# Kernel optimization log

Hardware: AMD Instinct MI355X
Metric: run time of the kernel (lower is better)

Reference implementation:

```python
import jax, jax.numpy as jnp
import numpy as np

DIM = 512
BATCH = 4096
STEPS = 30
GOVERNOR_RANK = 321
LAMBDA_0 = 15.045
RANK_EPS = 1e-5


def setup_inputs() -> dict:
    key = jax.random.key(0)
    kx, kw = jax.random.split(key)
    x = jax.random.normal(kx, (BATCH, DIM), dtype=jnp.float32)
    # nn.Linear(dim, dim) with weight ~ N(0, (1.2/sqrt(dim))^2), bias = 0.01
    std = 1.2 / float(np.sqrt(DIM))
    W = jax.random.normal(kw, (DIM, DIM), dtype=jnp.float32) * std
    b = jnp.full((DIM,), 0.01, dtype=jnp.float32)
    return {"x": x, "W": W, "b": b}


def reference(x, W, b):
    # is_governed = governor_rank < 1e6 -> True, so the amplify branch is dead code.
    norm_factor = float(np.sqrt(BATCH * DIM))
    k = min(BATCH, DIM)  # number of singular values from thin SVD
    idx = jnp.arange(k)

    def step(h, _):
        h = h @ W.T + b  # [B, D]
        U, S, Vh = jnp.linalg.svd(h, full_matrices=False)  # U:[B,k] S:[k] Vh:[k,D]
        current_rank = jnp.sum(S > RANK_EPS)
        trunc = current_rank > GOVERNOR_RANK
        S = jnp.where(trunc & (idx >= GOVERNOR_RANK), 0.0, S)
        l1_sings = jnp.sum(S) / norm_factor  # recorded BEFORE rescale, as in torch
        scale = jnp.where(l1_sings > LAMBDA_0,
                          LAMBDA_0 * norm_factor / jnp.sum(S), 1.0)
        h = (U * (S * scale)) @ Vh  # reconstruct U diag(S) Vh
        return h, l1_sings

    _, activations = jax.lax.scan(step, x, None, length=STEPS)
    return activations  # [STEPS] l1 singular-value sums, matching the returned list
```

## Files before the change

### kernel.cpp

```cpp
#include <hip/hip_runtime.h>
#include <math.h>

#define DIM 512
#define BATCH 4096
#define NSTEPS 30
#define KEEP 321

#define S_BETA 0
#define S_SCALE 1
#define S_VTV 4
#define S_SC 5

#define TDG 32
#define MTAIL 96

__device__ __forceinline__ double wred(double v) {
#pragma unroll
  for (int o = 32; o > 0; o >>= 1) v += __shfl_down(v, (unsigned)o, 64);
  return v;
}

__device__ __forceinline__ void stg(double* p, double v) {
  __hip_atomic_store(p, v, __ATOMIC_RELAXED, __HIP_MEMORY_SCOPE_AGENT);
}
__device__ __forceinline__ double ldg_(const double* p) {
  return __hip_atomic_load(p, __ATOMIC_RELAXED, __HIP_MEMORY_SCOPE_AGENT);
}

__device__ __forceinline__ void gbar2(unsigned* __restrict__ flags, unsigned& gen) {
  gen++;
  const unsigned target = gen;
  __syncthreads();
  if (threadIdx.x == 0) {
    __threadfence();
    __hip_atomic_store(flags + (size_t)blockIdx.x * 32, target, __ATOMIC_RELAXED, __HIP_MEMORY_SCOPE_AGENT);
  }
  if (threadIdx.x < 64) {
    bool ok = ((int)threadIdx.x >= TDG);
    while (!__all(ok)) {
      if (!ok) {
        unsigned v = __hip_atomic_load(flags + (size_t)threadIdx.x * 32, __ATOMIC_RELAXED, __HIP_MEMORY_SCOPE_AGENT);
        ok = (v >= target);
      }
    }
    __threadfence();
  }
  __syncthreads();
}

__device__ __forceinline__ void gbarf(unsigned* __restrict__ flags, unsigned& gen) {
  gen++;
  const unsigned target = gen;
  __syncthreads();
  if (threadIdx.x == 0) {
    __hip_atomic_store(flags + (size_t)blockIdx.x * 32, target, __ATOMIC_RELAXED, __HIP_MEMORY_SCOPE_AGENT);
  }
  if (threadIdx.x < 64) {
    bool ok = ((int)threadIdx.x >= TDG);
    while (!__all(ok)) {
      if (!ok) {
        unsigned v = __hip_atomic_load(flags + (size_t)threadIdx.x * 32, __ATOMIC_RELAXED, __HIP_MEMORY_SCOPE_AGENT);
        ok = (v >= target);
      }
    }
    asm volatile("" ::: "memory");
  }
  __syncthreads();
}


__global__ __launch_bounds__(256) void k_cast(const float* __restrict__ W, const float* __restrict__ b,
                                              double* __restrict__ Wd, double* __restrict__ bd,
                                              unsigned* __restrict__ cflags) {
  int idx = blockIdx.x * 256 + threadIdx.x;
  if (idx < DIM * DIM) Wd[idx] = (double)W[idx];
  if (idx < DIM) bd[idx] = (double)b[idx];
  if (blockIdx.x == 0) {
    for (int i = threadIdx.x; i < 1024; i += 256) cflags[i] = 0;
  }
}

__global__ __launch_bounds__(512) void k_colsum(const float* __restrict__ x, double* __restrict__ mvec) {
  int j = threadIdx.x;
  double s = 0.0;
  for (int r = 0; r < BATCH; ++r) s += (double)x[(size_t)r * DIM + j];
  mvec[j] = s;
}

__global__ __launch_bounds__(256) void k_xtx(const float* __restrict__ x, double* __restrict__ Gx) {
  __shared__ double As[16][65];
  __shared__ double Bs[16][65];
  const int tid = threadIdx.x;
  const int tx = tid & 15, ty = tid >> 4;
  const int bi = blockIdx.y * 64, bj = blockIdx.x * 64;
  const int lr = tid >> 4, lc4 = (tid & 15) * 4;
  double acc[4][4] = {};
  for (int r0 = 0; r0 < BATCH; r0 += 16) {
#pragma unroll
    for (int q = 0; q < 4; ++q) {
      As[lr][lc4 + q] = (double)x[(size_t)(r0 + lr) * DIM + bi + lc4 + q];
      Bs[lr][lc4 + q] = (double)x[(size_t)(r0 + lr) * DIM + bj + lc4 + q];
    }
    __syncthreads();
#pragma unroll
    for (int rr = 0; rr < 16; ++rr) {
      double a[4], bb[4];
#pragma unroll
      for (int u = 0; u < 4; ++u) a[u] = As[rr][ty * 4 + u];
#pragma unroll
      for (int v = 0; v < 4; ++v) bb[v] = Bs[rr][tx * 4 + v];
#pragma unroll
      for (int u = 0; u < 4; ++u)
#pragma unroll
        for (int v = 0; v < 4; ++v) acc[u][v] += a[u] * bb[v];
    }
    __syncthreads();
  }
#pragma unroll
  for (int u = 0; u < 4; ++u)
#pragma unroll
    for (int v = 0; v < 4; ++v) Gx[(size_t)(bi + ty * 4 + u) * DIM + bj + tx * 4 + v] = acc[u][v];
}

__global__ __launch_bounds__(256) void k_chol_mw(const double* __restrict__ G, double* __restrict__ R,
                                                 unsigned* __restrict__ flags) {
  __shared__ double Lr[16][512];
  __shared__ double rowk[512];
  const int tid = threadIdx.x, lane = tid & 63, wid = tid >> 6;
  const int g = blockIdx.x;
  unsigned gen = 0;
  for (int s = 0; s < 16; ++s) {
    const int i = s * 32 + g;
    for (int j = tid; j < DIM; j += 256) Lr[s][j] = G[(size_t)i * DIM + j];
  }
  __syncthreads();
  for (int k = 0; k < DIM; ++k) {
    if ((k & 31) == g) {
      const int s = k >> 5;
      double dkk = Lr[s][k];
      double sq = sqrt(fmax(dkk, 1e-280));
      double inv = 1.0 / sq;
      for (int j = tid; j < DIM; j += 256) {
        double v;
        if (j < k) v = 0.0;
        else if (j == k) v = sq;
        else v = Lr[s][j] * inv;
        stg(&R[(size_t)k * DIM + j], v);
      }
    }
    gbarf(flags, gen);
    for (int j = k + tid; j < DIM; j += 256) rowk[j] = ldg_(&R[(size_t)k * DIM + j]);
    __syncthreads();
    for (int s = wid; s < 16; s += 4) {
      const int i = s * 32 + g;
      if (i <= k) continue;
      const double rki = rowk[i];
      for (int j = i + lane; j < DIM; j += 64) Lr[s][j] -= rki * rowk[j];
    }
    __syncthreads();
  }
}

__global__ __launch_bounds__(64) void k_solvec0(const double* __restrict__ R, const double* __restrict__ mvec,
                                                double* __restrict__ c0) {
  const int lane = threadIdx.x;
  double rhs[8], cs[8];
#pragma unroll
  for (int r = 0; r < 8; ++r) rhs[r] = mvec[lane + 64 * r];
#pragma unroll
  for (int r = 0; r < 8; ++r) cs[r] = 0.0;
  for (int i = 0; i < DIM; ++i) {
    int owner = i & 63, ri = i >> 6;
    double ci = 0.0;
    if (lane == owner) {
      ci = rhs[ri] / R[(size_t)i * DIM + i];
      cs[ri] = ci;
    }
    ci = __shfl(ci, owner, 64);
    const double* row = R + (size_t)i * DIM;
#pragma unroll
    for (int r = 0; r < 8; ++r) {
      int j = lane + 64 * r;
      if (j > i) rhs[r] -= ci * row[j];
    }
  }
#pragma unroll
  for (int r = 0; r < 8; ++r) c0[lane + 64 * r] = cs[r];
}


__global__ __launch_bounds__(512) void k_prep(const double* __restrict__ cstv, const double* __restrict__ bd, int r,
                                              double* __restrict__ tvec, double* __restrict__ Mm,
                                              double* __restrict__ scal, unsigned* __restrict__ tflags) {
  __shared__ double redb[8];
  __shared__ double bc[1];
  const int tid = threadIdx.x, lane = tid & 63, wid = tid >> 6;
  for (int i = tid; i < 1024; i += 512) tflags[i] = 0;
  double p = 0.0;
  for (int i = tid; i < r; i += 512) {
    double c = cstv[i];
    p += c * c;
    tvec[i] = c;
  }
  p = wred(p);
  if (lane == 0) redb[wid] = p;
  __syncthreads();
  if (tid == 0) {
    double s = 0;
    for (int q = 0; q < 8; ++q) s += redb[q];
    double beta = sqrt(fmax(4096.0 - s, 1e-20));
    tvec[r] = beta;
    scal[S_BETA] = beta;
    bc[0] = beta;
  }
  __syncthreads();
  double beta = bc[0];
  for (int j = tid; j < DIM; j += 512) Mm[(size_t)r * DIM + j] = beta * bd[j];
}

__global__ __launch_bounds__(256) void k_gemm_nt(const double* __restrict__ A, const double* __restrict__ B,
                                                 double* __restrict__ C, int M, int N, int Kd, int lda, int ldb, int ldc,
                                                 const double* __restrict__ ur, const double* __restrict__ vr) {
  __shared__ double As[16][65];
  __shared__ double Bs[16][65];
  const int tid = threadIdx.x;
  const int tx = tid & 15, ty = tid >> 4;
  const int bi = blockIdx.y * 64, bj = blockIdx.x * 64;
  const int li = tid >> 2, lk = (tid & 3) * 4;
  double acc[4][4] = {};
  for (int k0 = 0; k0 < Kd; k0 += 16) {
    int gi = bi + li;
    bool oa = (gi < M);
    const double* pa = A + (size_t)(oa ? gi : 0) * lda + k0 + lk;
    int gj = bj + li;
    bool ob = (gj < N);
    const double* pb = B + (size_t)(ob ? gj : 0) * ldb + k0 + lk;
#pragma unroll
    for (int q = 0; q < 4; ++q) {
      int gk = k0 + lk + q;
      As[lk + q][li] = (oa && gk < Kd) ? pa[q] : 0.0;
      Bs[lk + q][li] = (ob && gk < Kd) ? pb[q] : 0.0;
    }
    __syncthreads();
#pragma unroll
    for (int kk = 0; kk < 16; ++kk) {
      double a[4], bb[4];
#pragma unroll
      for (int u = 0; u < 4; ++u) a[u] = As[kk][ty * 4 + u];
#pragma unroll
      for (int v = 0; v < 4; ++v) bb[v] = Bs[kk][tx * 4 + v];
#pragma unroll
      for (int u = 0; u < 4; ++u)
#pragma unroll
        for (int v = 0; v < 4; ++v) acc[u][v] += a[u] * bb[v];
    }
    __syncthreads();
  }
#pragma unroll
  for (int u = 0; u < 4; ++u) {
    int gi = bi + ty * 4 + u;
    if (gi >= M) continue;
#pragma unroll
    for (int v = 0; v < 4; ++v) {
      int gj = bj + tx * 4 + v;
      if (gj >= N) continue;
      double val = acc[u][v];
      if (ur) val += ur[gi] * vr[gj];
      C[(size_t)gi * ldc + gj] = val;
    }
  }
}

__global__ __launch_bounds__(256) void k_syrk(const double* __restrict__ M, double* __restrict__ C, int n, int Kd,
                                              int ld, int ldc) {
  __shared__ double As[16][65];
  __shared__ double Bs[16][65];
  int bid = blockIdx.x;
  int by = 0;
  while ((by + 1) * (by + 2) / 2 <= bid) by++;
  int bx = bid - by * (by + 1) / 2;
  const int tid = threadIdx.x;
  const int tx = tid & 15, ty = tid >> 4;
  const int bi = by * 64, bj = bx * 64;
  const int li = tid >> 2, lk = (tid & 3) * 4;
  double acc[4][4] = {};
  for (int k0 = 0; k0 < Kd; k0 += 16) {
    int gi = bi + li;
    bool oa = (gi < n);
    const double* pa = M + (size_t)(oa ? gi : 0) * ld + k0 + lk;
    int gj = bj + li;
    bool ob = (gj < n);
    const double* pb = M + (size_t)(ob ? gj : 0) * ld + k0 + lk;
#pragma unroll
    for (int q = 0; q < 4; ++q) {
      As[lk + q][li] = oa ? pa[q] : 0.0;
      Bs[lk + q][li] = ob ? pb[q] : 0.0;
    }
    __syncthreads();
#pragma unroll
    for (int kk = 0; kk < 16; ++kk) {
      double a[4], bb[4];
#pragma unroll
      for (int u = 0; u < 4; ++u) a[u] = As[kk][ty * 4 + u];
#pragma unroll
      for (int v = 0; v < 4; ++v) bb[v] = Bs[kk][tx * 4 + v];
#pragma unroll
      for (int u = 0; u < 4; ++u)
#pragma unroll
        for (int v = 0; v < 4; ++v) acc[u][v] += a[u] * bb[v];
    }
    __syncthreads();
  }
#pragma unroll
  for (int u = 0; u < 4; ++u) {
    int gi = bi + ty * 4 + u;
    if (gi >= n) continue;
#pragma unroll
    for (int v = 0; v < 4; ++v) {
      int gj = bj + tx * 4 + v;
      if (gj >= n) continue;
      double val = acc[u][v];
      C[(size_t)gi * ldc + gj] = val;
      if (by > bx) C[(size_t)gj * ldc + gi] = val;
    }
  }
}

__global__ __launch_bounds__(256) void k_tridiag_mw(double* __restrict__ A, int n, double* __restrict__ d,
                                                    double* __restrict__ e, double* __restrict__ tau,
                                                    double* __restrict__ Vrow, double* __restrict__ pvec,
                                                    double* __restrict__ orow, double* __restrict__ vtpp,
                                                    unsigned* __restrict__ flags) {
  __shared__ double vsh[520];
  __shared__ double wsh[520];
  __shared__ double xsh[520];
  __shared__ double redb[4];
  __shared__ double redb2[4];
  __shared__ double bc[1];
  const int tid = threadIdx.x, lane = tid & 63, wid = tid >> 6;
  const int g = blockIdx.x;
  unsigned gen = 0;
  const int ktail = n - 1 - MTAIL;
  double dval = A[0];
  for (int i = tid; i < n - 1; i += 256) xsh[i] = A[1 + i];
  __syncthreads();
  for (int k = 0; k < ktail; ++k) {
    const int m = n - 1 - k;
    const int par = k & 1;
    double* __restrict__ pv = pvec + par * 520;
    double* __restrict__ orw = orow + par * 520;
    double* __restrict__ vt = vtpp + par * 32;
    double part = 0.0;
    for (int i = tid; i < m; i += 256) {
      double xi = xsh[i];
      part += xi * xi;
    }
    part = wred(part);
    if (lane == 0) redb[wid] = part;
    __syncthreads();
    double s2 = redb[0] + redb[1] + redb[2] + redb[3];
    double x0 = xsh[0];
    double tk, v0, alpha;
    if (s2 < 1e-260) {
      tk = 0.0;
      v0 = 0.0;
      alpha = x0;
    } else {
      double sig = sqrt(s2);
      alpha = (x0 >= 0.0) ? -sig : sig;
      v0 = x0 - alpha;
      double vn2 = s2 - x0 * x0 + v0 * v0;
      tk = 2.0 / vn2;
    }
    for (int i = tid; i < m; i += 256) vsh[i] = (i == 0) ? v0 : xsh[i];
    __syncthreads();
    if (g == 0 && tid == 0) {
      d[k] = dval;
      e[k] = alpha;
      tau[k] = tk;
    }
    {
      double* __restrict__ Vr = Vrow + (size_t)k * n;
      for (int i = g * 256 + tid; i < m; i += TDG * 256) Vr[i] = vsh[i];
    }
    if (((k + 1) & (TDG - 1)) == g) {
      const double* __restrict__ rk1 = A + (size_t)(k + 1) * n + (k + 1);
      for (int j = tid; j < m; j += 256) stg(&orw[j], rk1[j]);
    }
    const int rem = (k + 1) & (TDG - 1);
    const int r0 = (k + 1) + ((g - rem + TDG) & (TDG - 1));
    double vtp = 0.0;
    for (int r = r0 + wid * TDG; r < n; r += 4 * TDG) {
      const int i = r - (k + 1);
      const double* __restrict__ row = A + (size_t)r * n + (k + 1);
      double acc = 0.0;
      for (int j = lane; j < m; j += 64) acc += row[j] * vsh[j];
      acc = wred(acc);
      if (lane == 0) {
        double pi = tk * acc;
        stg(&pv[i], pi);
        vtp += vsh[i] * pi;
      }
    }
    if (lane == 0) redb2[wid] = vtp;
    __syncthreads();
    if (tid == 0) stg(&vt[g], redb2[0] + redb2[1] + redb2[2] + redb2[3]);
    gbarf(flags, gen);
    if (wid == 0) {
      double vv = (lane < TDG) ? ldg_(&vt[lane]) : 0.0;
      vv = wred(vv);
      if (lane == 0) bc[0] = vv;
    }
    __syncthreads();
    const double K0 = 0.5 * tk * bc[0];
    for (int i = tid; i < m; i += 256) wsh[i] = ldg_(&pv[i]) - K0 * vsh[i];
    __syncthreads();
    const double w0 = wsh[0], vv0 = vsh[0];
    for (int i = tid; i < m - 1; i += 256) xsh[i] = ldg_(&orw[i + 1]) - vsh[i + 1] * w0 - wsh[i + 1] * vv0;
    if (tid == 0) dval = ldg_(&orw[0]) - 2.0 * vv0 * w0;
    for (int r = r0 + wid * TDG; r < n; r += 4 * TDG) {
      const int i = r - (k + 1);
      const double vi = vsh[i], wi = wsh[i];
      double* __restrict__ row = A + (size_t)r * n + (k + 1);
      for (int j = lane; j < m; j += 64) row[j] -= vi * wsh[j] + wi * vsh[j];
    }
    __syncthreads();
  }
  gbar2(flags, gen);
  if (g != 0) return;
  for (int k = ktail; k <= n - 3; ++k) {
    const int m = n - 1 - k;
    double part = 0.0;
    for (int i = tid; i < m; i += 256) {
      double xi = xsh[i];
      vsh[i] = xi;
      part += xi * xi;
    }
    part = wred(part);
    if (lane == 0) redb[wid] = part;
    __syncthreads();
    double s2 = redb[0] + redb[1] + redb[2] + redb[3];
    double x0 = vsh[0];
    double tk, v0, alpha;
    if (s2 < 1e-260) {
      tk = 0.0;
      v0 = 0.0;
      alpha = x0;
    } else {
      double sig = sqrt(s2);
      alpha = (x0 >= 0.0) ? -sig : sig;
      v0 = x0 - alpha;
      double vn2 = s2 - x0 * x0 + v0 * v0;
      tk = 2.0 / vn2;
    }
    __syncthreads();
    if (tid == 0) {
      vsh[0] = v0;
      d[k] = A[(size_t)k * n + k];
      e[k] = alpha;
      tau[k] = tk;
    }
    __syncthreads();
    double* __restrict__ Vr = Vrow + (size_t)k * n;
    for (int i = tid; i < m; i += 256) Vr[i] = vsh[i];
    double vtp = 0.0;
    for (int i = wid; i < m; i += 4) {
      const double* __restrict__ row = A + (size_t)(k + 1 + i) * n + (k + 1);
      double acc = 0.0;
      for (int j = lane; j < m; j += 64) acc += row[j] * vsh[j];
      acc = wred(acc);
      if (lane == 0) {
        double pi = tk * acc;
        wsh[i] = pi;
        vtp += vsh[i] * pi;
      }
    }
    if (lane == 0) redb2[wid] = vtp;
    __syncthreads();
    const double K0 = 0.5 * tk * (redb2[0] + redb2[1] + redb2[2] + redb2[3]);
    for (int i = wid; i < m; i += 4) {
      const double vi = vsh[i];
      const double ci = wsh[i] - 2.0 * K0 * vsh[i];
      double* __restrict__ row = A + (size_t)(k + 1 + i) * n + (k + 1);
      for (int j = lane; j < m; j += 64) {
        double nv = row[j] - (vi * wsh[j] + ci * vsh[j]);
        row[j] = nv;
        if (j == 0 && i >= 1) xsh[i - 1] = nv;
      }
    }
    __syncthreads();
  }
  if (tid == 0) {
    d[n - 2] = A[(size_t)(n - 2) * n + (n - 2)];
    e[n - 2] = A[(size_t)(n - 1) * n + (n - 2)];
    d[n - 1] = A[(size_t)(n - 1) * n + (n - 1)];
  }
}

__global__ __launch_bounds__(64) void k_bisect_mw(const double* __restrict__ d, const double* __restrict__ e, int n,
                                                  double* __restrict__ lam) {
  __shared__ double ds[520];
  __shared__ double e2s[520];
  __shared__ double bc[4];
  const int tid = threadIdx.x;
  for (int i = tid; i < n; i += 64) {
    ds[i] = d[i];
    e2s[i] = (i >= 1) ? e[i - 1] * e[i - 1] : 0.0;
  }
  __syncthreads();
  if (tid == 0) {
    double glo = 1e300, ghi = -1e300, me2 = 0.0;
    for (int i = 0; i < n; ++i) {
      double ea = (i >= 1) ? sqrt(e2s[i]) : 0.0;
      double eb = (i < n - 1) ? sqrt(e2s[i + 1]) : 0.0;
      glo = fmin(glo, ds[i] - ea - eb);
      ghi = fmax(ghi, ds[i] + ea + eb);
      me2 = fmax(me2, e2s[i]);
    }
    double span = ghi - glo;
    bc[0] = glo - 1e-3 * span - 1e-30;
    bc[1] = ghi + 1e-3 * span + 1e-30;
    bc[2] = fmax(me2 * 2.220446049250313e-16, 1e-280);
  }
  __syncthreads();
  const int idx = blockIdx.x * 64 + tid;
  if (idx < n) {
    double lo = bc[0], hi = bc[1];
    const double pivmin = bc[2];
    for (int r = 0; r < 34; ++r) {
      double x = 0.5 * (lo + hi);
      int cnt = 0;
      double q = ds[0] - x;
      if (q < 0.0) cnt++;
      for (int i = 1; i < n; ++i) {
        double t = q;
        if (fabs(t) < pivmin) t = (t < 0.0) ? -pivmin : pivmin;
        q = (ds[i] - x) - e2s[i] / t;
        if (q < 0.0) cnt++;
      }
      if (cnt <= idx) lo = x;
      else hi = x;
    }
    lam[idx] = 0.5 * (lo + hi);
  }
}

__global__ __launch_bounds__(64) void k_specsum(const double* __restrict__ lam, int n, int keep_start, int step,
                                                float* __restrict__ out, double* __restrict__ scal) {
  if (threadIdx.x == 0) {
    int cnt = 0;
    double st = 0.0, sa = 0.0;
    for (int i = 0; i < n; ++i) {
      double l = lam[i];
      double s = (l > 0.0) ? sqrt(l) : 0.0;
      if (s > 1e-5) cnt++;
      sa += s;
      if (i >= keep_start) st += s;
    }
    bool trunc = (cnt > 321);
    double ssum = trunc ? st : sa;
    const double NORMF = 1448.1546878700494;
    double l1 = ssum / NORMF;
    out[step] = (float)l1;
    scal[S_SCALE] = (l1 > 15.045) ? (15.045 / l1) : 1.0;
  }
}

__global__ __launch_bounds__(512) void k_eigvec(const double* __restrict__ Vrow, int n, const double* __restrict__ d,
                                                const double* __restrict__ e, const double* __restrict__ tau,
                                                const double* __restrict__ lam, const double* __restrict__ Mm,
                                                const double* __restrict__ tvec, double* __restrict__ scal,
                                                double* __restrict__ vhh, double* __restrict__ g) {
  __shared__ double zs[384];
  __shared__ double cps[384];
  __shared__ double dsh[384];
  __shared__ double esh[384];
  __shared__ double tsh[384];
  __shared__ double tvsh[384];
  __shared__ double bc[2];
  const int tid = threadIdx.x;
  for (int i = tid; i < n; i += 512) {
    dsh[i] = d[i];
    esh[i] = e[i];
    tsh[i] = tau[i];
    tvsh[i] = tvec[i];
  }
  __syncthreads();
  if (tid == 0) {
    double lmax = fabs(lam[n - 1]);
    double sh = lam[0] - (1e-12 * lmax + 1e-280);
    double me2 = 0.0;
    for (int i = 1; i < n; ++i) {
      double t = esh[i - 1];
      me2 = fmax(me2, t * t);
    }
    double pivmin = fmax(me2 * 2.220446049250313e-16, 1e-280);
    unsigned s = 0xB5297A4Du;
    for (int i = 0; i < n; ++i) {
      s = s * 1664525u + 1013904223u;
      zs[i] = 0.75 + (double)(s >> 8) * (0.5 / 16777216.0);
    }
    for (int it = 0; it < 3; ++it) {
      double den = dsh[0] - sh;
      if (fabs(den) < pivmin) den = (den < 0) ? -pivmin : pivmin;
      cps[0] = esh[0] / den;
      zs[0] = zs[0] / den;
      for (int i = 1; i < n; ++i) {
        den = (dsh[i] - sh) - esh[i - 1] * cps[i - 1];
        if (fabs(den) < pivmin) den = (den < 0) ? -pivmin : pivmin;
        cps[i] = (i < n - 1) ? esh[i] / den : 0.0;
        zs[i] = (zs[i] - esh[i - 1] * zs[i - 1]) / den;
      }
      for (int i = n - 2; i >= 0; --i) zs[i] -= cps[i] * zs[i + 1];
      double nn = 0;
      for (int i = 0; i < n; ++i) nn += zs[i] * zs[i];
      double inv = 1.0 / sqrt(fmax(nn, 1e-300));
      for (int i = 0; i < n; ++i) zs[i] *= inv;
    }
  }
  __syncthreads();
  if (tid < 64) {
    double z[6];
#pragma unroll
    for (int r = 0; r < 6; ++r) {
      int j = tid + 64 * r;
      z[r] = (j < n) ? zs[j] : 0.0;
    }
    for (int k = n - 3; k >= 0; --k) {
      const double tk = tsh[k];
      const double* __restrict__ vr = Vrow + (size_t)k * n;
      double vv[6];
#pragma unroll
      for (int r = 0; r < 6; ++r) {
        int j = tid + 64 * r;
        vv[r] = (j >= k + 1 && j < n) ? vr[j - k - 1] : 0.0;
      }
      double p = 0.0;
#pragma unroll
      for (int r = 0; r < 6; ++r) p += vv[r] * z[r];
      p = wred(p);
      p = __shfl(p, 0, 64);
      double tp = tk * p;
#pragma unroll
      for (int r = 0; r < 6; ++r) z[r] -= tp * vv[r];
    }
    double nn = 0.0;
#pragma unroll
    for (int r = 0; r < 6; ++r) nn += z[r] * z[r];
    nn = wred(nn);
    nn = __shfl(nn, 0, 64);
    double inv = 1.0 / sqrt(fmax(nn, 1e-300));
#pragma unroll
    for (int r = 0; r < 6; ++r) {
      int j = tid + 64 * r;
      if (j < n) zs[j] = z[r] * inv;
    }
  }
  __syncthreads();
  if (tid == 0) {
    double wl = zs[n - 1];
    double sg = (wl >= 0.0) ? 1.0 : -1.0;
    double coef = 1.0 / (1.0 + fabs(wl));
    zs[n - 1] = wl + sg;
    scal[S_VTV] = 2.0 + 2.0 * fabs(wl);
    bc[0] = coef;
    double sc = 0.0;
    for (int i = 0; i < n; ++i) sc += zs[i] * tvsh[i];
    scal[S_SC] = sc * coef;
  }
  __syncthreads();
  const double coef = bc[0];
  {
    double acc = 0.0;
    for (int i = 0; i < n; ++i) acc += zs[i] * Mm[(size_t)i * DIM + tid];
    g[tid] = coef * acc;
  }
  for (int i = tid; i < n; i += 512) vhh[i] = zs[i];
}

__global__ __launch_bounds__(512) void k_ii_multi(const double* __restrict__ d, const double* __restrict__ e,
                                                  const double* __restrict__ lam, int n, int keep_start,
                                                  double* __restrict__ Uk, double* __restrict__ cp) {
  const int tid = threadIdx.x, lane = tid & 63, wid = tid >> 6;
  __shared__ double redb[8];
  __shared__ double bc[1];
  if (tid < KEEP) {
    int j = tid;
    double lj = lam[keep_start + j];
    double me2 = 0.0;
    for (int i = 1; i < n; ++i) {
      double t = e[i - 1];
      me2 = fmax(me2, t * t);
    }
    double pivmin = fmax(me2 * 2.220446049250313e-16, 1e-280);
    unsigned s = 0x9E3779B9u * (unsigned)(j + 13);
    for (int i = 0; i < n; ++i) {
      s = s * 1664525u + 1013904223u;
      Uk[(size_t)i * KEEP + j] = 0.5 + (double)(s >> 8) * (1.0 / 16777216.0);
    }
    for (int it = 0; it < 3; ++it) {
      double den = d[0] - lj;
      if (fabs(den) < pivmin) den = (den < 0.0) ? -pivmin : pivmin;
      double cprev = e[0] / den;
      cp[0 * KEEP + j] = cprev;
      double zprev = Uk[0 * KEEP + j] / den;
      Uk[0 * KEEP + j] = zprev;
      for (int i = 1; i < n; ++i) {
        den = (d[i] - lj) - e[i - 1] * cprev;
        if (fabs(den) < pivmin) den = (den < 0.0) ? -pivmin : pivmin;
        double ci = (i < n - 1) ? e[i] / den : 0.0;
        cp[(size_t)i * KEEP + j] = ci;
        double zi = (Uk[(size_t)i * KEEP + j] - e[i - 1] * zprev) / den;
        Uk[(size_t)i * KEEP + j] = zi;
        zprev = zi;
        cprev = ci;
      }
      double zn = Uk[(size_t)(n - 1) * KEEP + j];
      for (int i = n - 2; i >= 0; --i) {
        zn = Uk[(size_t)i * KEEP + j] - cp[(size_t)i * KEEP + j] * zn;
        Uk[(size_t)i * KEEP + j] = zn;
      }
      double nn = 0;
      for (int i = 0; i < n; ++i) {
        double z = Uk[(size_t)i * KEEP + j];
        nn += z * z;
      }
      double inv = 1.0 / sqrt(fmax(nn, 1e-300));
      for (int i = 0; i < n; ++i) Uk[(size_t)i * KEEP + j] *= inv;
    }
  }
  __syncthreads();
  for (int jj = 1; jj < KEEP; ++jj) {
    double l1v = lam[keep_start + jj], l0v = lam[keep_start + jj - 1];
    bool close = (l1v - l0v) < 1e-7 * (fabs(l1v) + 1e-280);
    if (!close) continue;
    double p = 0;
    for (int i = tid; i < n; i += 512) p += Uk[(size_t)i * KEEP + jj] * Uk[(size_t)i * KEEP + jj - 1];
    p = wred(p);
    if (lane == 0) redb[wid] = p;
    __syncthreads();
    if (tid == 0) {
      double s2 = 0;
      for (int q = 0; q < 8; ++q) s2 += redb[q];
      bc[0] = s2;
    }
    __syncthreads();
    double dot = bc[0];
    for (int i = tid; i < n; i += 512) Uk[(size_t)i * KEEP + jj] -= dot * Uk[(size_t)i * KEEP + jj - 1];
    __syncthreads();
    p = 0;
    for (int i = tid; i < n; i += 512) {
      double z = Uk[(size_t)i * KEEP + jj];
      p += z * z;
    }
    p = wred(p);
    if (lane == 0) redb[wid] = p;
    __syncthreads();
    if (tid == 0) {
      double s2 = 0;
      for (int q = 0; q < 8; ++q) s2 += redb[q];
      bc[0] = 1.0 / sqrt(fmax(s2, 1e-300));
    }
    __syncthreads();
    double inv = bc[0];
    for (int i = tid; i < n; i += 512) Uk[(size_t)i * KEEP + jj] *= inv;
    __syncthreads();
  }
}

__global__ __launch_bounds__(64) void k_hhapply_multi(const double* __restrict__ Vrow, const double* __restrict__ tau,
                                                      int n, double* __restrict__ Uk) {
  const int j = blockIdx.x;
  const int lane = threadIdx.x;
  for (int k = n - 3; k >= 0; --k) {
    double tk = tau[k];
    if (tk == 0.0) continue;
    int m = n - 1 - k;
    const double* __restrict__ vr = Vrow + (size_t)k * n;
    double p = 0.0;
    for (int i = lane; i < m; i += 64) p += vr[i] * Uk[(size_t)(k + 1 + i) * KEEP + j];
    p = wred(p);
    p = __shfl(p, 0, 64);
    double tp = tk * p;
    for (int i = lane; i < m; i += 64) Uk[(size_t)(k + 1 + i) * KEEP + j] -= tp * vr[i];
  }
  double nn = 0.0;
  for (int i = lane; i < n; i += 64) {
    double z = Uk[(size_t)i * KEEP + j];
    nn += z * z;
  }
  nn = wred(nn);
  nn = __shfl(nn, 0, 64);
  double inv = 1.0 / sqrt(fmax(nn, 1e-300));
  for (int i = lane; i < n; i += 64) Uk[(size_t)i * KEEP + j] *= inv;
}

__global__ __launch_bounds__(256) void k_gemm_tn(const double* __restrict__ A, const double* __restrict__ B,
                                                 double* __restrict__ C, int M, int N, int Kd, int lda, int ldb, int ldc,
                                                 const double* __restrict__ scal) {
  __shared__ double As[16][65];
  __shared__ double Bs[16][65];
  const int tid = threadIdx.x;
  const int tx = tid & 15, ty = tid >> 4;
  const int bi = blockIdx.y * 64, bj = blockIdx.x * 64;
  const int li = tid & 63, lq = tid >> 6;
  double acc[4][4] = {};
  for (int k0 = 0; k0 < Kd; k0 += 16) {
#pragma unroll
    for (int q = 0; q < 4; ++q) {
      int kk = lq + q * 4;
      int gk = k0 + kk;
      int gi = bi + li;
      int gj = bj + li;
      As[kk][li] = (gi < M && gk < Kd) ? A[(size_t)gk * lda + gi] : 0.0;
      Bs[kk][li] = (gj < N && gk < Kd) ? B[(size_t)gk * ldb + gj] : 0.0;
    }
    __syncthreads();
#pragma unroll
    for (int kk = 0; kk < 16; ++kk) {
      double a[4], bb[4];
#pragma unroll
      for (int u = 0; u < 4; ++u) a[u] = As[kk][ty * 4 + u];
#pragma unroll
      for (int v = 0; v < 4; ++v) bb[v] = Bs[kk][tx * 4 + v];
#pragma unroll
      for (int u = 0; u < 4; ++u)
#pragma unroll
        for (int v = 0; v < 4; ++v) acc[u][v] += a[u] * bb[v];
    }
    __syncthreads();
  }
  double s = scal[S_SCALE];
#pragma unroll
  for (int u = 0; u < 4; ++u) {
    int gi = bi + ty * 4 + u;
    if (gi >= M) continue;
#pragma unroll
    for (int v = 0; v < 4; ++v) {
      int gj = bj + tx * 4 + v;
      if (gj >= N) continue;
      C[(size_t)gi * ldc + gj] = s * acc[u][v];
    }
  }
}

__global__ __launch_bounds__(512) void k_gemv_tn(const double* __restrict__ Uk, const double* __restrict__ tvec,
                                                 double* __restrict__ cstv, int n) {
  int i = threadIdx.x;
  if (i < KEEP) {
    double acc = 0.0;
    for (int k = 0; k < n; ++k) acc += Uk[(size_t)k * KEEP + i] * tvec[k];
    cstv[i] = acc;
  }
}

__global__ __launch_bounds__(256) void k_hh_update(const double* __restrict__ Mm, const double* __restrict__ vhh,
                                                   const double* __restrict__ g, const double* __restrict__ scal,
                                                   const double* __restrict__ tvec, double* __restrict__ Cst,
                                                   double* __restrict__ cstv) {
  int idx = blockIdx.x * 256 + threadIdx.x;
  double scale = scal[S_SCALE];
  if (idx < KEEP * DIM) {
    int i = idx >> 9, j = idx & 511;
    Cst[(size_t)i * DIM + j] = scale * (Mm[(size_t)i * DIM + j] - vhh[i] * g[j]);
  }
  if (blockIdx.x == 0 && threadIdx.x < KEEP) {
    cstv[threadIdx.x] = tvec[threadIdx.x] - vhh[threadIdx.x] * scal[S_SC];
  }
}


extern "C" void kernel_launch(void* const* d_in, const int* in_sizes, int n_in, void* d_out, int out_size, void* d_ws,
                              size_t ws_size, hipStream_t stream) {
  (void)in_sizes;
  (void)n_in;
  (void)out_size;
  (void)ws_size;
  const float* x = (const float*)d_in[0];
  const float* W = (const float*)d_in[1];
  const float* b = (const float*)d_in[2];
  float* out = (float*)d_out;

  char* ws = (char*)d_ws;
  size_t off = 0;
  auto alloc = [&](size_t nelem) {
    size_t p = off;
    off += (nelem * 8 + 255) & ~(size_t)255;
    return (double*)(ws + p);
  };
  double* Wd = alloc(512 * 512);
  double* bd = alloc(512);
  double* mvec = alloc(512);
  double* Cst = alloc(512 * 512);
  double* cstv = alloc(520);
  double* tvec = alloc(520);
  double* Mm = alloc(513 * 512);
  double* AwGx = alloc(513 * 513);
  double* Gx = AwGx;
  double* Aw = AwGx;
  double* zcp = AwGx;
  double* Vrow = alloc(513 * 513);
  double* dT = alloc(520);
  double* eT = alloc(520);
  double* tauT = alloc(520);
  double* lam = alloc(520);
  double* vhh = alloc(520);
  double* gv = alloc(520);
  double* scal = alloc(32);
  double* Uk = alloc(513 * 321);
  double* pvec = alloc(1040);
  double* orow = alloc(1040);
  double* vtpp = alloc(64);
  unsigned* tflags = (unsigned*)alloc(512);
  unsigned* cflags = (unsigned*)alloc(512);

  k_cast<<<dim3((512 * 512 + 255) / 256), dim3(256), 0, stream>>>(W, b, Wd, bd, cflags);
  k_colsum<<<dim3(1), dim3(512), 0, stream>>>(x, mvec);
  k_xtx<<<dim3(8, 8), dim3(256), 0, stream>>>(x, Gx);
  k_chol_mw<<<dim3(TDG), dim3(256), 0, stream>>>(Gx, Cst, cflags);
  k_solvec0<<<dim3(1), dim3(64), 0, stream>>>(Cst, mvec, cstv);

  {
    const int r = 512, n = 513;
    k_prep<<<dim3(1), dim3(512), 0, stream>>>(cstv, bd, r, tvec, Mm, scal, tflags);
    k_gemm_nt<<<dim3(8, 8), dim3(256), 0, stream>>>(Cst, Wd, Mm, r, 512, 512, 512, 512, 512, cstv, bd);
    k_syrk<<<dim3(45), dim3(256), 0, stream>>>(Mm, Aw, n, 512, 512, n);
    k_tridiag_mw<<<dim3(TDG), dim3(256), 0, stream>>>(Aw, n, dT, eT, tauT, Vrow, pvec, orow, vtpp, tflags);
    k_bisect_mw<<<dim3((n + 63) / 64), dim3(64), 0, stream>>>(dT, eT, n, lam);
    k_specsum<<<dim3(1), dim3(64), 0, stream>>>(lam, n, n - KEEP, 0, out, scal);
    k_ii_multi<<<dim3(1), dim3(512), 0, stream>>>(dT, eT, lam, n, n - KEEP, Uk, zcp);
    k_hhapply_multi<<<dim3(KEEP), dim3(64), 0, stream>>>(Vrow, tauT, n, Uk);
    k_gemm_tn<<<dim3(8, 6), dim3(256), 0, stream>>>(Uk, Mm, Cst, KEEP, 512, n, KEEP, 512, 512, scal);
    k_gemv_tn<<<dim3(1), dim3(512), 0, stream>>>(Uk, tvec, cstv, n);
  }

  for (int t = 1; t < NSTEPS; ++t) {
    const int r = KEEP, n = KEEP + 1;
    k_prep<<<dim3(1), dim3(512), 0, stream>>>(cstv, bd, r, tvec, Mm, scal, tflags);
    k_gemm_nt<<<dim3(8, 6), dim3(256), 0, stream>>>(Cst, Wd, Mm, r, 512, 512, 512, 512, 512, cstv, bd);
    k_syrk<<<dim3(21), dim3(256), 0, stream>>>(Mm, Aw, n, 512, 512, n);
    k_tridiag_mw<<<dim3(TDG), dim3(256), 0, stream>>>(Aw, n, dT, eT, tauT, Vrow, pvec, orow, vtpp, tflags);
    k_bisect_mw<<<dim3((n + 63) / 64), dim3(64), 0, stream>>>(dT, eT, n, lam);
    k_specsum<<<dim3(1), dim3(64), 0, stream>>>(lam, n, 1, t, out, scal);
    k_eigvec<<<dim3(1), dim3(512), 0, stream>>>(Vrow, n, dT, eT, tauT, lam, Mm, tvec, scal, vhh, gv);
    k_hh_update<<<dim3((KEEP * DIM + 255) / 256), dim3(256), 0, stream>>>(Mm, vhh, gv, scal, tvec, Cst, cstv);
  }
}
```

Baseline: 126.0 ms.

## Block Householder tridiagonalization with delayed rank-2k trailing updates (panel of 8)

Converts the multi-block Householder tridiagonalization from per-column rank-2 trailing updates to a blocked, LAPACK sytrd-style scheme. Panels of 8 reflectors are accumulated in shared-memory V/W buffers, the matvec is corrected using those buffers, and the trailing matrix is written back once per panel. This cuts global-memory read-modify-write passes over the matrix and removes the separate next-row broadcast buffer. The single-block tail is enlarged from 96 to 160 columns. The cost is extra per-step correction dot products, more shared memory, and tricky coherence for rows read before the panel update has been applied.

```diff
diff --git a/kernel.cpp b/kernel.cpp
--- a/kernel.cpp
+++ b/kernel.cpp
@@ -12,7 +12,8 @@
 #define S_SC 5
 
 #define TDG 32
-#define MTAIL 96
+#define NB 8
+#define MTAIL 160
 
 __device__ __forceinline__ double wred(double v) {
 #pragma unroll
@@ -329,110 +330,169 @@
 __global__ __launch_bounds__(256) void k_tridiag_mw(double* __restrict__ A, int n, double* __restrict__ d,
                                                     double* __restrict__ e, double* __restrict__ tau,
                                                     double* __restrict__ Vrow, double* __restrict__ pvec,
-                                                    double* __restrict__ orow, double* __restrict__ vtpp,
-                                                    unsigned* __restrict__ flags) {
-  __shared__ double vsh[520];
-  __shared__ double wsh[520];
-  __shared__ double xsh[520];
+                                                    double* __restrict__ vtpp, unsigned* __restrict__ flags) {
+  __shared__ double Vp[NB][524];
+  __shared__ double Wp[NB][524];
+  __shared__ double xsh[524];
+  __shared__ double xt[MTAIL + 8];
   __shared__ double redb[4];
   __shared__ double redb2[4];
+  __shared__ double cvw[2 * NB];
   __shared__ double bc[1];
   const int tid = threadIdx.x, lane = tid & 63, wid = tid >> 6;
   const int g = blockIdx.x;
   unsigned gen = 0;
   const int ktail = n - 1 - MTAIL;
   double dval = A[0];
-  for (int i = tid; i < n - 1; i += 256) xsh[i] = A[1 + i];
-  __syncthreads();
-  for (int k = 0; k < ktail; ++k) {
-    const int m = n - 1 - k;
-    const int par = k & 1;
-    double* __restrict__ pv = pvec + par * 520;
-    double* __restrict__ orw = orow + par * 520;
-    double* __restrict__ vt = vtpp + par * 32;
-    double part = 0.0;
-    for (int i = tid; i < m; i += 256) {
-      double xi = xsh[i];
-      part += xi * xi;
-    }
-    part = wred(part);
-    if (lane == 0) redb[wid] = part;
-    __syncthreads();
-    double s2 = redb[0] + redb[1] + redb[2] + redb[3];
-    double x0 = xsh[0];
-    double tk, v0, alpha;
-    if (s2 < 1e-260) {
-      tk = 0.0;
-      v0 = 0.0;
-      alpha = x0;
-    } else {
-      double sig = sqrt(s2);
-      alpha = (x0 >= 0.0) ? -sig : sig;
-      v0 = x0 - alpha;
-      double vn2 = s2 - x0 * x0 + v0 * v0;
-      tk = 2.0 / vn2;
-    }
-    for (int i = tid; i < m; i += 256) vsh[i] = (i == 0) ? v0 : xsh[i];
-    __syncthreads();
-    if (g == 0 && tid == 0) {
-      d[k] = dval;
-      e[k] = alpha;
-      tau[k] = tk;
-    }
+  for (int r = 1 + tid; r < n; r += 256) xsh[r] = A[r];
+  __syncthreads();
+
+  for (int k0 = 0; k0 < ktail; k0 += NB) {
+    const int pw = min(NB, ktail - k0);
+    const int b0 = k0 + 1;
+    const int m0 = n - b0;
+    for (int l = 0; l < NB; ++l)
+      for (int c = tid; c < m0; c += 256) {
+        Vp[l][c] = 0.0;
+        Wp[l][c] = 0.0;
+      }
+    __syncthreads();
+
+    for (int j = 0; j < pw; ++j) {
+      const int k = k0 + j;
+      const int m = m0 - j;
+      const int par = k & 1;
+      double* __restrict__ pv = pvec + par * 520;
+      double* __restrict__ vt = vtpp + par * 32;
+      double* __restrict__ vsh = Vp[j];
+      double* __restrict__ wsh = Wp[j];
+      double part = 0.0;
+      for (int r = k + 1 + tid; r < n; r += 256) part += xsh[r] * xsh[r];
+      part = wred(part);
+      if (lane == 0) redb[wid] = part;
+      __syncthreads();
+      double s2 = redb[0] + redb[1] + redb[2] + redb[3];
+      double x0 = xsh[k + 1];
+      double tk, v0, alpha;
+      if (s2 < 1e-260) {
+        tk = 0.0;
+        v0 = 0.0;
+        alpha = x0;
+      } else {
+        double sig = sqrt(s2);
+        alpha = (x0 >= 0.0) ? -sig : sig;
+        v0 = x0 - alpha;
+        double vn2 = s2 - x0 * x0 + v0 * v0;
+        tk = 2.0 / vn2;
+      }
+      for (int c = j + tid; c < m0; c += 256) vsh[c] = (c == j) ? v0 : xsh[b0 + c];
+      __syncthreads();
+      if (g == 0 && tid == 0) {
+        d[k] = dval;
+        e[k] = alpha;
+        tau[k] = tk;
+      }
+      {
+        double* __restrict__ Vr = Vrow + (size_t)k * n;
+        for (int i = g * 256 + tid; i < m; i += TDG * 256) Vr[i] = vsh[j + i];
+      }
+      if (tid >= 2 * j && tid < 2 * NB) cvw[tid] = 0.0;
+      for (int t = wid; t < 2 * j; t += 4) {
+        const int l = t >> 1;
+        const double* __restrict__ src = (t & 1) ? Vp[l] : Wp[l];
+        double acc = 0.0;
+        for (int c = j + lane; c < m0; c += 64) acc += src[c] * vsh[c];
+        acc = wred(acc);
+        if (lane == 0) cvw[t] = acc;
+      }
+      __syncthreads();
+      const int rem = (k + 1) & (TDG - 1);
+      const int r0 = (k + 1) + ((g - rem + TDG) & (TDG - 1));
+      double vtp = 0.0;
+      for (int r = r0 + wid * TDG; r < n; r += 4 * TDG) {
+        const int cr = r - b0;
+        const int i = r - (k + 1);
+        const double* __restrict__ row = A + (size_t)r * n + b0;
+        double acc = 0.0;
+        for (int c = j + lane; c < m0; c += 64) acc += row[c] * vsh[c];
+        acc = wred(acc);
+        if (lane == 0) {
+          double corr = 0.0;
+#pragma unroll
+          for (int l = 0; l < NB; ++l) corr += Vp[l][cr] * cvw[2 * l] + Wp[l][cr] * cvw[2 * l + 1];
+          double pi = tk * (acc - corr);
+          stg(&pv[i], pi);
+          vtp += vsh[cr] * pi;
+        }
+      }
+      if (lane == 0) redb2[wid] = vtp;
+      __syncthreads();
+      if (tid == 0) stg(&vt[g], redb2[0] + redb2[1] + redb2[2] + redb2[3]);
+      gbarf(flags, gen);
+      if (wid == 0) {
+        double vv = (lane < TDG) ? ldg_(&vt[lane]) : 0.0;
+        vv = wred(vv);
+        if (lane == 0) bc[0] = vv;
+      }
+      __syncthreads();
+      const double K0 = 0.5 * tk * bc[0];
+      for (int c = j + tid; c < m0; c += 256) wsh[c] = ldg_(&pv[c - j]) - K0 * vsh[c];
+      __syncthreads();
+      {
+        const double* __restrict__ srow = A + (size_t)(k + 1) * n + b0;
+        for (int c = j + 1 + tid; c < m0; c += 256) {
+          double acc = ldg_(&srow[c]);
+#pragma unroll
+          for (int l = 0; l < NB; ++l) acc -= Vp[l][j] * Wp[l][c] + Wp[l][j] * Vp[l][c];
+          xsh[b0 + c] = acc;
+        }
+        if (tid == 0) {
+          double acc = ldg_(&srow[j]);
+#pragma unroll
+          for (int l = 0; l < NB; ++l) acc -= 2.0 * Vp[l][j] * Wp[l][j];
+          dval = acc;
+        }
+      }
+      __syncthreads();
+    }
+
     {
-      double* __restrict__ Vr = Vrow + (size_t)k * n;
-      for (int i = g * 256 + tid; i < m; i += TDG * 256) Vr[i] = vsh[i];
-    }
-    if (((k + 1) & (TDG - 1)) == g) {
-      const double* __restrict__ rk1 = A + (size_t)(k + 1) * n + (k + 1);
-      for (int j = tid; j < m; j += 256) stg(&orw[j], rk1[j]);
-    }
-    const int rem = (k + 1) & (TDG - 1);
-    const int r0 = (k + 1) + ((g - rem + TDG) & (TDG - 1));
-    double vtp = 0.0;
-    for (int r = r0 + wid * TDG; r < n; r += 4 * TDG) {
-      const int i = r - (k + 1);
-      const double* __restrict__ row = A + (size_t)r * n + (k + 1);
-      double acc = 0.0;
-      for (int j = lane; j < m; j += 64) acc += row[j] * vsh[j];
-      acc = wred(acc);
-      if (lane == 0) {
-        double pi = tk * acc;
-        stg(&pv[i], pi);
-        vtp += vsh[i] * pi;
-      }
-    }
-    if (lane == 0) redb2[wid] = vtp;
-    __syncthreads();
-    if (tid == 0) stg(&vt[g], redb2[0] + redb2[1] + redb2[2] + redb2[3]);
-    gbarf(flags, gen);
-    if (wid == 0) {
-      double vv = (lane < TDG) ? ldg_(&vt[lane]) : 0.0;
-      vv = wred(vv);
-      if (lane == 0) bc[0] = vv;
-    }
-    __syncthreads();
-    const double K0 = 0.5 * tk * bc[0];
-    for (int i = tid; i < m; i += 256) wsh[i] = ldg_(&pv[i]) - K0 * vsh[i];
-    __syncthreads();
-    const double w0 = wsh[0], vv0 = vsh[0];
-    for (int i = tid; i < m - 1; i += 256) xsh[i] = ldg_(&orw[i + 1]) - vsh[i + 1] * w0 - wsh[i + 1] * vv0;
-    if (tid == 0) dval = ldg_(&orw[0]) - 2.0 * vv0 * w0;
-    for (int r = r0 + wid * TDG; r < n; r += 4 * TDG) {
-      const int i = r - (k + 1);
-      const double vi = vsh[i], wi = wsh[i];
-      double* __restrict__ row = A + (size_t)r * n + (k + 1);
-      for (int j = lane; j < m; j += 64) row[j] -= vi * wsh[j] + wi * vsh[j];
-    }
-    __syncthreads();
-  }
+      const int kend = k0 + pw;
+      const int rem = (kend + 1) & (TDG - 1);
+      const int r0 = (kend + 1) + ((g - rem + TDG) & (TDG - 1));
+      for (int r = r0 + wid * TDG; r < n; r += 4 * TDG) {
+        const int cr = r - b0;
+        double vlr[NB], wlr[NB];
+#pragma unroll
+        for (int l = 0; l < NB; ++l) {
+          vlr[l] = Vp[l][cr];
+          wlr[l] = Wp[l][cr];
+        }
+        double* __restrict__ row = A + (size_t)r * n + b0;
+        const bool wt = (r <= kend + NB);
+        for (int c = pw + lane; c < m0; c += 64) {
+          double a = row[c];
+#pragma unroll
+          for (int l = 0; l < NB; ++l) a -= vlr[l] * Wp[l][c] + wlr[l] * Vp[l][c];
+          row[c] = a;
+          if (wt) stg(&row[c], a);
+        }
+      }
+    }
+    __syncthreads();
+  }
+
   gbar2(flags, gen);
   if (g != 0) return;
+  for (int i = tid; i < n - 1 - ktail; i += 256) xt[i] = xsh[ktail + 1 + i];
+  double* __restrict__ vsh = Vp[0];
+  double* __restrict__ wsh = Wp[0];
+  __syncthreads();
   for (int k = ktail; k <= n - 3; ++k) {
     const int m = n - 1 - k;
     double part = 0.0;
     for (int i = tid; i < m; i += 256) {
-      double xi = xsh[i];
+      double xi = xt[i];
       vsh[i] = xi;
       part += xi * xi;
     }
@@ -456,7 +516,7 @@
     __syncthreads();
     if (tid == 0) {
       vsh[0] = v0;
-      d[k] = A[(size_t)k * n + k];
+      d[k] = (k == ktail) ? dval : A[(size_t)k * n + k];
       e[k] = alpha;
       tau[k] = tk;
     }
@@ -485,7 +545,7 @@
       for (int j = lane; j < m; j += 64) {
         double nv = row[j] - (vi * wsh[j] + ci * vsh[j]);
         row[j] = nv;
-        if (j == 0 && i >= 1) xsh[i - 1] = nv;
+        if (j == 0 && i >= 1) xt[i - 1] = nv;
       }
     }
     __syncthreads();
@@ -909,7 +969,6 @@
   double* scal = alloc(32);
   double* Uk = alloc(513 * 321);
   double* pvec = alloc(1040);
-  double* orow = alloc(1040);
   double* vtpp = alloc(64);
   unsigned* tflags = (unsigned*)alloc(512);
   unsigned* cflags = (unsigned*)alloc(512);
@@ -925,7 +984,7 @@
     k_prep<<<dim3(1), dim3(512), 0, stream>>>(cstv, bd, r, tvec, Mm, scal, tflags);
     k_gemm_nt<<<dim3(8, 8), dim3(256), 0, stream>>>(Cst, Wd, Mm, r, 512, 512, 512, 512, 512, cstv, bd);
     k_syrk<<<dim3(45), dim3(256), 0, stream>>>(Mm, Aw, n, 512, 512, n);
-    k_tridiag_mw<<<dim3(TDG), dim3(256), 0, stream>>>(Aw, n, dT, eT, tauT, Vrow, pvec, orow, vtpp, tflags);
+    k_tridiag_mw<<<dim3(TDG), dim3(256), 0, stream>>>(Aw, n, dT, eT, tauT, Vrow, pvec, vtpp, tflags);
     k_bisect_mw<<<dim3((n + 63) / 64), dim3(64), 0, stream>>>(dT, eT, n, lam);
     k_specsum<<<dim3(1), dim3(64), 0, stream>>>(lam, n, n - KEEP, 0, out, scal);
     k_ii_multi<<<dim3(1), dim3(512), 0, stream>>>(dT, eT, lam, n, n - KEEP, Uk, zcp);
@@ -939,7 +998,7 @@
     k_prep<<<dim3(1), dim3(512), 0, stream>>>(cstv, bd, r, tvec, Mm, scal, tflags);
     k_gemm_nt<<<dim3(8, 6), dim3(256), 0, stream>>>(Cst, Wd, Mm, r, 512, 512, 512, 512, 512, cstv, bd);
     k_syrk<<<dim3(21), dim3(256), 0, stream>>>(Mm, Aw, n, 512, 512, n);
-    k_tridiag_mw<<<dim3(TDG), dim3(256), 0, stream>>>(Aw, n, dT, eT, tauT, Vrow, pvec, orow, vtpp, tflags);
+    k_tridiag_mw<<<dim3(TDG), dim3(256), 0, stream>>>(Aw, n, dT, eT, tauT, Vrow, pvec, vtpp, tflags);
     k_bisect_mw<<<dim3((n + 63) / 64), dim3(64), 0, stream>>>(dT, eT, n, lam);
     k_specsum<<<dim3(1), dim3(64), 0, stream>>>(lam, n, 1, t, out, scal);
     k_eigvec<<<dim3(1), dim3(512), 0, stream>>>(Vrow, n, dT, eT, tauT, lam, Mm, tvec, scal, vhh, gv);
```

Result: slower. 184.6 ms (+46.5%).

## Use multisection bisection with one wavefront per eigenvalue; merge tridiag loops

Applied to the files above, without the earlier changes.

Eigenvalue bisection now gives each eigenvalue its own block of 64 lanes. Each lane evaluates a different Sturm count, so an interval narrows by a factor of 65 per round, and 7 rounds replace 34 serial bisection steps. Gershgorin bounds are reduced across the wavefront instead of computed serially by one thread. In the tridiagonalization, the w and x updates are fused into one loop, removing a block barrier per Householder step. The cost is far more total Sturm-count work, n blocks times 64 lanes times 7 rounds, and the final accuracy after 7 rounds of 65-way splitting is slightly different.

```diff
diff --git a/kernel.cpp b/kernel.cpp
--- a/kernel.cpp
+++ b/kernel.cpp
@@ -413,11 +413,15 @@
     }
     __syncthreads();
     const double K0 = 0.5 * tk * bc[0];
-    for (int i = tid; i < m; i += 256) wsh[i] = ldg_(&pv[i]) - K0 * vsh[i];
-    __syncthreads();
-    const double w0 = wsh[0], vv0 = vsh[0];
-    for (int i = tid; i < m - 1; i += 256) xsh[i] = ldg_(&orw[i + 1]) - vsh[i + 1] * w0 - wsh[i + 1] * vv0;
+    const double vv0 = vsh[0];
+    const double w0 = ldg_(&pv[0]) - K0 * vv0;
+    for (int i = tid; i < m; i += 256) {
+      double w = ldg_(&pv[i]) - K0 * vsh[i];
+      wsh[i] = w;
+      if (i >= 1) xsh[i - 1] = ldg_(&orw[i]) - vsh[i] * w0 - w * vv0;
+    }
     if (tid == 0) dval = ldg_(&orw[0]) - 2.0 * vv0 * w0;
+    __syncthreads();
     for (int r = r0 + wid * TDG; r < n; r += 4 * TDG) {
       const int i = r - (k + 1);
       const double vi = vsh[i], wi = wsh[i];
@@ -497,52 +501,57 @@
   }
 }
 
-__global__ __launch_bounds__(64) void k_bisect_mw(const double* __restrict__ d, const double* __restrict__ e, int n,
+__global__ __launch_bounds__(64) void k_bisect_ms(const double* __restrict__ d, const double* __restrict__ e, int n,
                                                   double* __restrict__ lam) {
   __shared__ double ds[520];
   __shared__ double e2s[520];
-  __shared__ double bc[4];
-  const int tid = threadIdx.x;
-  for (int i = tid; i < n; i += 64) {
+  const int lane = threadIdx.x;
+  const int ev = blockIdx.x;
+  for (int i = lane; i < n; i += 64) {
     ds[i] = d[i];
     e2s[i] = (i >= 1) ? e[i - 1] * e[i - 1] : 0.0;
   }
   __syncthreads();
-  if (tid == 0) {
-    double glo = 1e300, ghi = -1e300, me2 = 0.0;
-    for (int i = 0; i < n; ++i) {
-      double ea = (i >= 1) ? sqrt(e2s[i]) : 0.0;
-      double eb = (i < n - 1) ? sqrt(e2s[i + 1]) : 0.0;
-      glo = fmin(glo, ds[i] - ea - eb);
-      ghi = fmax(ghi, ds[i] + ea + eb);
-      me2 = fmax(me2, e2s[i]);
-    }
-    double span = ghi - glo;
-    bc[0] = glo - 1e-3 * span - 1e-30;
-    bc[1] = ghi + 1e-3 * span + 1e-30;
-    bc[2] = fmax(me2 * 2.220446049250313e-16, 1e-280);
-  }
-  __syncthreads();
-  const int idx = blockIdx.x * 64 + tid;
-  if (idx < n) {
-    double lo = bc[0], hi = bc[1];
-    const double pivmin = bc[2];
-    for (int r = 0; r < 34; ++r) {
-      double x = 0.5 * (lo + hi);
-      int cnt = 0;
-      double q = ds[0] - x;
+  double glo = 1e300, ghi = -1e300, me2 = 0.0;
+  for (int i = lane; i < n; i += 64) {
+    double ea = (i >= 1) ? sqrt(e2s[i]) : 0.0;
+    double eb = (i < n - 1) ? sqrt(e2s[i + 1]) : 0.0;
+    glo = fmin(glo, ds[i] - ea - eb);
+    ghi = fmax(ghi, ds[i] + ea + eb);
+    me2 = fmax(me2, e2s[i]);
+  }
+#pragma unroll
+  for (int o = 32; o > 0; o >>= 1) {
+    glo = fmin(glo, __shfl_down(glo, (unsigned)o, 64));
+    ghi = fmax(ghi, __shfl_down(ghi, (unsigned)o, 64));
+    me2 = fmax(me2, __shfl_down(me2, (unsigned)o, 64));
+  }
+  glo = __shfl(glo, 0, 64);
+  ghi = __shfl(ghi, 0, 64);
+  me2 = __shfl(me2, 0, 64);
+  double span = ghi - glo;
+  double lo = glo - 1e-3 * span - 1e-30;
+  double hi = ghi + 1e-3 * span + 1e-30;
+  const double pivmin = fmax(me2 * 2.220446049250313e-16, 1e-280);
+  for (int r = 0; r < 7; ++r) {
+    const double x = lo + (hi - lo) * ((double)(lane + 1) * (1.0 / 65.0));
+    int cnt = 0;
+    double q = ds[0] - x;
+    if (q < 0.0) cnt++;
+    for (int i = 1; i < n; ++i) {
+      double t = q;
+      if (fabs(t) < pivmin) t = (t < 0.0) ? -pivmin : pivmin;
+      q = (ds[i] - x) - e2s[i] / t;
       if (q < 0.0) cnt++;
-      for (int i = 1; i < n; ++i) {
-        double t = q;
-        if (fabs(t) < pivmin) t = (t < 0.0) ? -pivmin : pivmin;
-        q = (ds[i] - x) - e2s[i] / t;
-        if (q < 0.0) cnt++;
-      }
-      if (cnt <= idx) lo = x;
-      else hi = x;
-    }
-    lam[idx] = 0.5 * (lo + hi);
-  }
+    }
+    unsigned long long mask = __ballot(cnt <= ev);
+    int pc = (int)__popcll(mask);
+    double nlo = (pc > 0) ? __shfl(x, pc - 1, 64) : lo;
+    double nhi = (pc < 64) ? __shfl(x, pc, 64) : hi;
+    lo = nlo;
+    hi = nhi;
+  }
+  if (lane == 0) lam[ev] = 0.5 * (lo + hi);
 }
 
 __global__ __launch_bounds__(64) void k_specsum(const double* __restrict__ lam, int n, int keep_start, int step,
@@ -926,7 +935,7 @@
     k_gemm_nt<<<dim3(8, 8), dim3(256), 0, stream>>>(Cst, Wd, Mm, r, 512, 512, 512, 512, 512, cstv, bd);
     k_syrk<<<dim3(45), dim3(256), 0, stream>>>(Mm, Aw, n, 512, 512, n);
     k_tridiag_mw<<<dim3(TDG), dim3(256), 0, stream>>>(Aw, n, dT, eT, tauT, Vrow, pvec, orow, vtpp, tflags);
-    k_bisect_mw<<<dim3((n + 63) / 64), dim3(64), 0, stream>>>(dT, eT, n, lam);
+    k_bisect_ms<<<dim3(n), dim3(64), 0, stream>>>(dT, eT, n, lam);
     k_specsum<<<dim3(1), dim3(64), 0, stream>>>(lam, n, n - KEEP, 0, out, scal);
     k_ii_multi<<<dim3(1), dim3(512), 0, stream>>>(dT, eT, lam, n, n - KEEP, Uk, zcp);
     k_hhapply_multi<<<dim3(KEEP), dim3(64), 0, stream>>>(Vrow, tauT, n, Uk);
@@ -940,7 +949,7 @@
     k_gemm_nt<<<dim3(8, 6), dim3(256), 0, stream>>>(Cst, Wd, Mm, r, 512, 512, 512, 512, 512, cstv, bd);
     k_syrk<<<dim3(21), dim3(256), 0, stream>>>(Mm, Aw, n, 512, 512, n);
     k_tridiag_mw<<<dim3(TDG), dim3(256), 0, stream>>>(Aw, n, dT, eT, tauT, Vrow, pvec, orow, vtpp, tflags);
-    k_bisect_mw<<<dim3((n + 63) / 64), dim3(64), 0, stream>>>(dT, eT, n, lam);
+    k_bisect_ms<<<dim3(n), dim3(64), 0, stream>>>(dT, eT, n, lam);
     k_specsum<<<dim3(1), dim3(64), 0, stream>>>(lam, n, 1, t, out, scal);
     k_eigvec<<<dim3(1), dim3(512), 0, stream>>>(Vrow, n, dT, eT, tauT, lam, Mm, tvec, scal, vhh, gv);
     k_hh_update<<<dim3((KEEP * DIM + 255) / 256), dim3(256), 0, stream>>>(Mm, vhh, gv, scal, tvec, Cst, cstv);
```

Result: faster. 106.4 ms, median of 2 (-15.5%).
